# Optimization experiments

Measured on AMD Instinct MI355X. Metric: run time of the kernel, lower is better.

## Reference

```python
import jax, jax.numpy as jnp
import numpy as np

EMBED = 256
HEADS = 8
HEAD_DIM = 32
MLP_DIM = 1024
NEG = -1e9  # large negative in place of -inf so fully-deselected rows don't NaN
LN_EPS = 1e-5


def _layernorm(x, g, b):
    m = jnp.mean(x, axis=-1, keepdims=True)
    v = jnp.mean(jnp.square(x - m), axis=-1, keepdims=True)
    return (x - m) / jnp.sqrt(v + LN_EPS) * g + b


def setup_inputs() -> dict:
    key = jax.random.key(0)
    ks = jax.random.split(key, 16)
    b, s, d = 64, 360, EMBED
    sc = 0.02
    return {
        "x": jax.random.normal(ks[0], (b, s, d), dtype=jnp.float32),
        "attention_mask": jnp.zeros((b, 1, 1, s), dtype=jnp.float32),
        # TokenRouter.weight_predictor: Linear(256, 1)
        "wp_w": jax.random.normal(ks[1], (1, d), dtype=jnp.float32) * sc,
        "wp_b": jnp.zeros((1,), dtype=jnp.float32),
        # TokenRouter.aux_predictor: Linear(256,128) -> SiLU -> Linear(128,2)
        "a1_w": jax.random.normal(ks[2], (d // 2, d), dtype=jnp.float32) * sc,
        "a1_b": jnp.zeros((d // 2,), dtype=jnp.float32),
        "a2_w": jax.random.normal(ks[3], (2, d // 2), dtype=jnp.float32) * sc,
        "a2_b": jnp.zeros((2,), dtype=jnp.float32),
        # transformer block (pre-LN GPT2-style)
        "ln1_g": jnp.ones((d,), dtype=jnp.float32),
        "ln1_b": jnp.zeros((d,), dtype=jnp.float32),
        "wqkv": jax.random.normal(ks[4], (d, 3 * d), dtype=jnp.float32) * sc,
        "bqkv": jnp.zeros((3 * d,), dtype=jnp.float32),
        "wo": jax.random.normal(ks[5], (d, d), dtype=jnp.float32) * sc,
        "bo": jnp.zeros((d,), dtype=jnp.float32),
        "ln2_g": jnp.ones((d,), dtype=jnp.float32),
        "ln2_b": jnp.zeros((d,), dtype=jnp.float32),
        "w1": jax.random.normal(ks[6], (d, MLP_DIM), dtype=jnp.float32) * sc,
        "b1": jnp.zeros((MLP_DIM,), dtype=jnp.float32),
        "w2": jax.random.normal(ks[7], (MLP_DIM, d), dtype=jnp.float32) * sc,
        "b2": jnp.zeros((d,), dtype=jnp.float32),
    }


def reference(x, attention_mask, wp_w, wp_b, a1_w, a1_b, a2_w, a2_b,
              ln1_g, ln1_b, wqkv, bqkv, wo, bo, ln2_g, ln2_b, w1, b1, w2, b2):
    b, s, d = x.shape
    # --- router: per-token scalar weight ---
    weights = (x @ wp_w.T + wp_b).squeeze(-1)  # [b, s]
    # --- aux predictor selects tokens (eval path: argmax over 2 logits) ---
    h = jax.nn.silu(x @ a1_w.T + a1_b)
    aux_logits = h @ a2_w.T + a2_b            # [b, s, 2]
    sel = jnp.argmax(aux_logits, axis=-1).astype(bool)  # [b, s]
    # --- masked transformer block over the selected token subset.
    # Compacting tokens then attending == full-seq attention with deselected
    # keys masked out (LN/MLP/residual are position-wise), so vectorize:
    bias = attention_mask + jnp.where(sel, 0.0, NEG)[:, None, None, :]  # [b,1,1,s]
    hn = _layernorm(x, ln1_g, ln1_b)
    qkv = hn @ wqkv + bqkv
    q, k, v = jnp.split(qkv, 3, axis=-1)
    q = q.reshape(b, s, HEADS, HEAD_DIM)
    k = k.reshape(b, s, HEADS, HEAD_DIM)
    v = v.reshape(b, s, HEADS, HEAD_DIM)
    scores = jnp.einsum("bqhd,bkhd->bhqk", q, k) / np.sqrt(HEAD_DIM).astype(np.float32)
    scores = scores + bias                   # [b, h, s, s]
    attn = jax.nn.softmax(scores, axis=-1)
    ctx = jnp.einsum("bhqk,bkhd->bqhd", attn, v).reshape(b, s, d)
    h1 = x + (ctx @ wo + bo)
    h2n = _layernorm(h1, ln2_g, ln2_b)
    block_out = h1 + (jax.nn.gelu(h2n @ w1 + b1) @ w2 + b2)  # [b, s, d]
    # --- scatter-recombine: selected -> weighted block output, else passthrough
    out = jnp.where(sel[..., None], block_out * weights[..., None], x)
    avg_selected = jnp.sum(sel.astype(x.dtype)) / b
    return out, avg_selected
```

## Files before the change

kernel.cpp:

```cpp
#include <hip/hip_runtime.h>
#include <math.h>
#include <stdint.h>

#define TOKN 23040
#define BSZ 64
#define SEQ 360
#define DIM 256
#define NHD 8
#define HDD 32
#define MLPD 1024
#define NEGV -1e9f

typedef __attribute__((ext_vector_type(8))) short bf16x8;
typedef __attribute__((ext_vector_type(4))) float f32x4;

static __device__ __forceinline__ short f2bs(float f) {
  unsigned u = __builtin_bit_cast(unsigned, f);
  u += 0x7fffu + ((u >> 16) & 1u);
  return (short)(u >> 16);
}
static __device__ __forceinline__ float bf2f(short s) {
  unsigned u = ((unsigned)(unsigned short)s) << 16;
  return __builtin_bit_cast(float, u);
}
static __device__ __forceinline__ unsigned packbf(float a, float b) {
  return (unsigned)(unsigned short)f2bs(a) | ((unsigned)(unsigned short)f2bs(b) << 16);
}
static __device__ __forceinline__ void gl16(const short* g, short* l) {
  __builtin_amdgcn_global_load_lds(
      (const __attribute__((address_space(1))) unsigned int*)g,
      (__attribute__((address_space(3))) unsigned int*)l, 16, 0, 0);
}

__global__ __launch_bounds__(256) void mega_k(
    const float* __restrict__ x, const float* __restrict__ g,
    const float* __restrict__ b, const float* __restrict__ wpw,
    const float* __restrict__ wpb, short* __restrict__ outn,
    float* __restrict__ wout, float* __restrict__ outx,
    const float* __restrict__ a1w, const float* __restrict__ a1b,
    const float* __restrict__ a2w, const float* __restrict__ a2b,
    int* __restrict__ sel,
    const float* __restrict__ wqkv, const float* __restrict__ wo,
    const float* __restrict__ w1, const float* __restrict__ w2,
    short* __restrict__ wqkvt, short* __restrict__ wot,
    short* __restrict__ w1t, short* __restrict__ w2t) {
  __shared__ __align__(16) unsigned char smem[20992];
  int bid = blockIdx.x;
  int t = threadIdx.x;

  if (bid < 720) {
    float(*XT)[36] = (float(*)[36])smem;
    float(*WT)[128] = (float(*)[128])(smem + 4608);
    int m0 = bid * 32;
    int tx = t & 31, ty = t >> 5;
    float acc[4][4] = {};
    int r = t >> 3, c = (t & 7) * 4;
    int n2 = t >> 1, c2 = (t & 1) * 16;
    for (int k0 = 0; k0 < 256; k0 += 32) {
      float4 xa = *(const float4*)(x + (size_t)(m0 + r) * 256 + k0 + c);
      XT[c + 0][r] = xa.x; XT[c + 1][r] = xa.y; XT[c + 2][r] = xa.z; XT[c + 3][r] = xa.w;
#pragma unroll
      for (int j = 0; j < 4; j++) {
        float4 wv = *(const float4*)(a1w + (size_t)n2 * 256 + k0 + c2 + j * 4);
        WT[c2 + j * 4 + 0][n2] = wv.x;
        WT[c2 + j * 4 + 1][n2] = wv.y;
        WT[c2 + j * 4 + 2][n2] = wv.z;
        WT[c2 + j * 4 + 3][n2] = wv.w;
      }
      __syncthreads();
#pragma unroll 8
      for (int kk = 0; kk < 32; kk++) {
        float4 wv4 = *(const float4*)&WT[kk][tx * 4];
        float4 xv4 = *(const float4*)&XT[kk][ty * 4];
        float xr[4] = {xv4.x, xv4.y, xv4.z, xv4.w};
        float wr[4] = {wv4.x, wv4.y, wv4.z, wv4.w};
#pragma unroll
        for (int i = 0; i < 4; i++)
#pragma unroll
          for (int j = 0; j < 4; j++) acc[i][j] += xr[i] * wr[j];
      }
      __syncthreads();
    }
    float b1v[4], a20[4], a21[4];
#pragma unroll
    for (int j = 0; j < 4; j++) {
      int dim = tx * 4 + j;
      b1v[j] = a1b[dim];
      a20[j] = a2w[dim];
      a21[j] = a2w[128 + dim];
    }
    float bias0 = a2b[0], bias1 = a2b[1];
#pragma unroll
    for (int i = 0; i < 4; i++) {
      float l0 = 0.f, l1 = 0.f;
#pragma unroll
      for (int j = 0; j < 4; j++) {
        float v = acc[i][j] + b1v[j];
        float h = v / (1.f + expf(-v));
        l0 += h * a20[j];
        l1 += h * a21[j];
      }
#pragma unroll
      for (int o = 1; o < 32; o <<= 1) { l0 += __shfl_xor(l0, o); l1 += __shfl_xor(l1, o); }
      if (tx == 0) sel[m0 + ty * 4 + i] = (l1 + bias1 > l0 + bias0) ? 1 : 0;
    }
  } else if (bid < 1488) {
    float(*tile)[33] = (float(*)[33])smem;
    int b2 = bid - 720;
    const float* src;
    short* dst;
    int K, N, kt, nt;
    if (b2 < 192) {
      src = wqkv; dst = wqkvt; K = 256; N = 768; kt = b2 / 24; nt = b2 % 24;
    } else if (b2 < 256) {
      int bb = b2 - 192; src = wo; dst = wot; K = 256; N = 256; kt = bb >> 3; nt = bb & 7;
    } else if (b2 < 512) {
      int bb = b2 - 256; src = w1; dst = w1t; K = 256; N = 1024; kt = bb >> 5; nt = bb & 31;
    } else {
      int bb = b2 - 512; src = w2; dst = w2t; K = 1024; N = 256; kt = bb >> 3; nt = bb & 7;
    }
    int r = t >> 3, c4 = (t & 7) * 4;
    const float4 v = *(const float4*)(src + (size_t)(kt * 32 + r) * N + nt * 32 + c4);
    tile[c4 + 0][r] = v.x;
    tile[c4 + 1][r] = v.y;
    tile[c4 + 2][r] = v.z;
    tile[c4 + 3][r] = v.w;
    __syncthreads();
    union { short s[4]; uint2 u; } o;
    o.s[0] = f2bs(tile[r][c4 + 0]);
    o.s[1] = f2bs(tile[r][c4 + 1]);
    o.s[2] = f2bs(tile[r][c4 + 2]);
    o.s[3] = f2bs(tile[r][c4 + 3]);
    *(uint2*)(dst + (size_t)(nt * 32 + r) * K + kt * 32 + c4) = o.u;
  } else {
    int tok = (bid - 1488) * 4 + (t >> 6);
    int lane = t & 63;
    const float4 xv = *(const float4*)(x + (size_t)tok * DIM + lane * 4);
    *(float4*)(outx + (size_t)tok * DIM + lane * 4) = xv;
    float s = xv.x + xv.y + xv.z + xv.w;
    float s2 = xv.x * xv.x + xv.y * xv.y + xv.z * xv.z + xv.w * xv.w;
#pragma unroll
    for (int o = 1; o < 64; o <<= 1) { s += __shfl_xor(s, o); s2 += __shfl_xor(s2, o); }
    float m = s * (1.f / DIM);
    float var = fmaxf(s2 * (1.f / DIM) - m * m, 0.f);
    float rstd = rsqrtf(var + 1e-5f);
    float4 gv = *(const float4*)(g + lane * 4);
    float4 bv = *(const float4*)(b + lane * 4);
    uint2 pk;
    pk.x = packbf((xv.x - m) * rstd * gv.x + bv.x, (xv.y - m) * rstd * gv.y + bv.y);
    pk.y = packbf((xv.z - m) * rstd * gv.z + bv.z, (xv.w - m) * rstd * gv.w + bv.w);
    *(uint2*)(outn + (size_t)tok * DIM + lane * 4) = pk;
    float4 wv = *(const float4*)(wpw + lane * 4);
    float wd = xv.x * wv.x + xv.y * wv.y + xv.z * wv.z + xv.w * wv.w;
#pragma unroll
    for (int o = 1; o < 64; o <<= 1) wd += __shfl_xor(wd, o);
    if (lane == 0) wout[tok] = wd + wpb[0];
  }
}

__global__ __launch_bounds__(512) void scan_k(
    const int* __restrict__ sel, int* __restrict__ g_idx,
    int* __restrict__ startp, int* __restrict__ cntp,
    int* __restrict__ mtotp, float* __restrict__ outavg) {
  __shared__ int sc[512];
  __shared__ int red[8];
  int b = blockIdx.x, t = threadIdx.x;
  int lane = t & 63, wave = t >> 6;
  int part = 0;
  for (int i = t; i < b * SEQ; i += 512) part += sel[i];
#pragma unroll
  for (int o = 1; o < 64; o <<= 1) part += __shfl_xor(part, o);
  if (lane == 0) red[wave] = part;
  __syncthreads();
  int start = 0;
#pragma unroll
  for (int w = 0; w < 8; w++) start += red[w];
  __syncthreads();
  int flag = (t < SEQ) ? sel[b * SEQ + t] : 0;
  sc[t] = flag;
  __syncthreads();
  int val = flag;
  for (int off = 1; off < 512; off <<= 1) {
    int add = (t >= off) ? sc[t - off] : 0;
    __syncthreads();
    val += add;
    sc[t] = val;
    __syncthreads();
  }
  if (flag) g_idx[start + val - 1] = b * SEQ + t;
  if (t == 511) { startp[b] = start; cntp[b] = val; }
  if (b == 63) {
    int mt = start + sc[511];
    if (t == 0) { *mtotp = mt; outavg[0] = (float)mt / 64.0f; }
    int e = mt + 256;
    if (e > TOKN) e = TOKN;
    for (int i = mt + t; i < e; i += 512) g_idx[i] = 0;
  }
}

template <int MODE, int BN>
__global__ __launch_bounds__(256) void gemm128_k(
    const short* __restrict__ A, const short* __restrict__ Bt,
    const float* __restrict__ bias, const float* __restrict__ resf,
    const short* __restrict__ resb, const float* __restrict__ wgt,
    const int* __restrict__ g_idx, const int* __restrict__ mtotp,
    short* __restrict__ outb, float* __restrict__ outf, int Ndim, int Kdim) {
  int Mt = *mtotp;
  int m0 = blockIdx.y * 128;
  if (m0 >= Mt) return;
  __shared__ __align__(16) short As[2][128 * 32];
  __shared__ __align__(16) short Bs[2][BN * 32];
  constexpr int NJ = BN / 32;
  int n0 = blockIdx.x * BN;
  int t = threadIdx.x;
  int wave = t >> 6, lane = t & 63;
  int l15 = lane & 15, quad = lane >> 4;
  int wr = (wave >> 1) * 64, wc = (wave & 1) * (BN / 2);
  int r0 = t >> 2, c0 = (t & 3) * 8;
  long arA = (MODE == 0) ? g_idx[m0 + r0] : (m0 + r0);
  long arB = (MODE == 0) ? g_idx[m0 + 64 + r0] : (m0 + 64 + r0);
  const short* gA0 = A + arA * Kdim + c0;
  const short* gA1 = A + arB * Kdim + c0;
  const short* gB0 = Bt + (size_t)(n0 + r0) * Kdim + c0;
  const short* gB1 = Bt + (size_t)(n0 + 64 + r0) * Kdim + c0;
  int wbase = wave * 512;

  f32x4 acc[4][NJ];
#pragma unroll
  for (int i = 0; i < 4; i++)
#pragma unroll
    for (int j = 0; j < NJ; j++)
#pragma unroll
      for (int r = 0; r < 4; r++) acc[i][j][r] = 0.f;

  int nst = Kdim >> 5;
  gl16(gA0, As[0] + wbase);
  gl16(gA1, As[0] + 2048 + wbase);
  gl16(gB0, Bs[0] + wbase);
  if constexpr (BN == 128) gl16(gB1, Bs[0] + 2048 + wbase);
  __syncthreads();

  int buf = 0;
  for (int s = 0; s < nst; ++s) {
    if (s + 1 < nst) {
      int off = (s + 1) * 32;
      short* d = (buf ^ 1) ? &As[1][0] : &As[0][0];
      short* e = (buf ^ 1) ? &Bs[1][0] : &Bs[0][0];
      gl16(gA0 + off, d + wbase);
      gl16(gA1 + off, d + 2048 + wbase);
      gl16(gB0 + off, e + wbase);
      if constexpr (BN == 128) gl16(gB1 + off, e + 2048 + wbase);
    }
    const short* Ab = buf ? &As[1][0] : &As[0][0];
    const short* Bb = buf ? &Bs[1][0] : &Bs[0][0];
    bf16x8 af[4], bfr[NJ];
#pragma unroll
    for (int i = 0; i < 4; i++)
      af[i] = *(const bf16x8*)&Ab[(wr + i * 16 + l15) * 32 + quad * 8];
#pragma unroll
    for (int j = 0; j < NJ; j++)
      bfr[j] = *(const bf16x8*)&Bb[(wc + j * 16 + l15) * 32 + quad * 8];
#pragma unroll
    for (int i = 0; i < 4; i++)
#pragma unroll
      for (int j = 0; j < NJ; j++)
        acc[i][j] = __builtin_amdgcn_mfma_f32_16x16x32_bf16(af[i], bfr[j],
                                                            acc[i][j], 0, 0, 0);
    __syncthreads();
    buf ^= 1;
  }

#pragma unroll
  for (int i = 0; i < 4; i++) {
#pragma unroll
    for (int j = 0; j < NJ; j++) {
      int col = n0 + wc + j * 16 + l15;
      float bcol = bias[col];
#pragma unroll
      for (int r = 0; r < 4; r++) {
        int row = m0 + wr + i * 16 + quad * 4 + r;
        float v = acc[i][j][r] + bcol;
        size_t idx = (size_t)row * Ndim + col;
        if (MODE == 0) {
          outb[idx] = f2bs(v);
        } else if (MODE == 2) {
          float u = 0.7978845608028654f * (v + 0.044715f * v * v * v);
          float e = __expf(2.f * u);
          float th = 1.f - 2.f / (e + 1.f);
          outb[idx] = f2bs(0.5f * v * (1.f + th));
        } else {
          if (row < Mt) {
            int orig = g_idx[row];
            float o = (v + bf2f(resb[idx])) * wgt[orig];
            outf[(size_t)orig * 256 + col] = o;
          }
        }
      }
    }
  }
}

__global__ __launch_bounds__(256) void wo_ln_k(
    const short* __restrict__ A, const short* __restrict__ Bt,
    const float* __restrict__ bias, const float* __restrict__ resf,
    const float* __restrict__ g2, const float* __restrict__ b2,
    const int* __restrict__ g_idx, const int* __restrict__ mtotp,
    short* __restrict__ h1b, short* __restrict__ h2n) {
  int Mt = *mtotp;
  int m0 = blockIdx.x * 128;
  if (m0 >= Mt) return;
  __shared__ __align__(16) short As0[128 * 32];
  __shared__ __align__(16) short As1[128 * 32];
  __shared__ __align__(16) short Bs0[256 * 32];
  __shared__ __align__(16) short Bs1[256 * 32];
  __shared__ float ps[128][2], ps2[128][2];
  int t = threadIdx.x;
  int wave = t >> 6, lane = t & 63;
  int l15 = lane & 15, quad = lane >> 4;
  int wr = (wave >> 1) * 64, wc = (wave & 1) * 128;
  int r0 = t >> 2, c0 = (t & 3) * 8;
  const short* gA0 = A + (size_t)(m0 + r0) * 256 + c0;
  const short* gA1 = A + (size_t)(m0 + 64 + r0) * 256 + c0;
  const short* gB0 = Bt + (size_t)r0 * 256 + c0;
  short* lA0 = As0 + wave * 512;
  short* lA1 = As1 + wave * 512;
  short* lB0 = Bs0 + wave * 512;
  short* lB1 = Bs1 + wave * 512;

  f32x4 acc[4][8];
#pragma unroll
  for (int i = 0; i < 4; i++)
#pragma unroll
    for (int j = 0; j < 8; j++)
#pragma unroll
      for (int r = 0; r < 4; r++) acc[i][j][r] = 0.f;

  for (int k0 = 0; k0 < 256; k0 += 64) {
    gl16(gA0 + k0, lA0);
    gl16(gA1 + k0, lA0 + 2048);
    gl16(gA0 + k0 + 32, lA1);
    gl16(gA1 + k0 + 32, lA1 + 2048);
#pragma unroll
    for (int q = 0; q < 4; q++) {
      gl16(gB0 + (size_t)q * 64 * 256 + k0, lB0 + q * 2048);
      gl16(gB0 + (size_t)q * 64 * 256 + k0 + 32, lB1 + q * 2048);
    }
    __syncthreads();
    bf16x8 af[4], bfr[8];
#pragma unroll
    for (int i = 0; i < 4; i++)
      af[i] = *(const bf16x8*)&As0[(wr + i * 16 + l15) * 32 + quad * 8];
#pragma unroll
    for (int j = 0; j < 8; j++)
      bfr[j] = *(const bf16x8*)&Bs0[(wc + j * 16 + l15) * 32 + quad * 8];
#pragma unroll
    for (int i = 0; i < 4; i++)
#pragma unroll
      for (int j = 0; j < 8; j++)
        acc[i][j] = __builtin_amdgcn_mfma_f32_16x16x32_bf16(af[i], bfr[j],
                                                            acc[i][j], 0, 0, 0);
#pragma unroll
    for (int i = 0; i < 4; i++)
      af[i] = *(const bf16x8*)&As1[(wr + i * 16 + l15) * 32 + quad * 8];
#pragma unroll
    for (int j = 0; j < 8; j++)
      bfr[j] = *(const bf16x8*)&Bs1[(wc + j * 16 + l15) * 32 + quad * 8];
#pragma unroll
    for (int i = 0; i < 4; i++)
#pragma unroll
      for (int j = 0; j < 8; j++)
        acc[i][j] = __builtin_amdgcn_mfma_f32_16x16x32_bf16(af[i], bfr[j],
                                                            acc[i][j], 0, 0, 0);
    __syncthreads();
  }

  float bcol[8], gcol[8], bbcol[8];
#pragma unroll
  for (int j = 0; j < 8; j++) {
    int col = wc + j * 16 + l15;
    bcol[j] = bias[col];
    gcol[j] = g2[col];
    bbcol[j] = b2[col];
  }
  float s1v[4][4], s2v[4][4];
#pragma unroll
  for (int i = 0; i < 4; i++) {
#pragma unroll
    for (int r = 0; r < 4; r++) {
      int row = m0 + wr + i * 16 + quad * 4 + r;
      int orig = g_idx[row];
      const float* xr = resf + (size_t)orig * 256;
      float ls_ = 0.f, ls2_ = 0.f;
#pragma unroll
      for (int j = 0; j < 8; j++) {
        int col = wc + j * 16 + l15;
        float h1 = acc[i][j][r] + bcol[j] + xr[col];
        acc[i][j][r] = h1;
        h1b[(size_t)row * 256 + col] = f2bs(h1);
        ls_ += h1;
        ls2_ += h1 * h1;
      }
      s1v[i][r] = ls_;
      s2v[i][r] = ls2_;
    }
  }
#pragma unroll
  for (int i = 0; i < 4; i++)
#pragma unroll
    for (int r = 0; r < 4; r++) {
#pragma unroll
      for (int o = 1; o < 16; o <<= 1) {
        s1v[i][r] += __shfl_xor(s1v[i][r], o);
        s2v[i][r] += __shfl_xor(s2v[i][r], o);
      }
    }
  if (l15 == 0) {
#pragma unroll
    for (int i = 0; i < 4; i++)
#pragma unroll
      for (int r = 0; r < 4; r++) {
        int lr = wr + i * 16 + quad * 4 + r;
        ps[lr][wave & 1] = s1v[i][r];
        ps2[lr][wave & 1] = s2v[i][r];
      }
  }
  __syncthreads();
#pragma unroll
  for (int i = 0; i < 4; i++) {
#pragma unroll
    for (int r = 0; r < 4; r++) {
      int lr = wr + i * 16 + quad * 4 + r;
      float S = ps[lr][0] + ps[lr][1];
      float S2 = ps2[lr][0] + ps2[lr][1];
      float m = S * (1.f / 256.f);
      float var = fmaxf(S2 * (1.f / 256.f) - m * m, 0.f);
      float rstd = rsqrtf(var + 1e-5f);
      int row = m0 + lr;
#pragma unroll
      for (int j = 0; j < 8; j++) {
        int col = wc + j * 16 + l15;
        float h2 = (acc[i][j][r] - m) * rstd * gcol[j] + bbcol[j];
        h2n[(size_t)row * 256 + col] = f2bs(h2);
      }
    }
  }
}

__global__ __launch_bounds__(256) void attn_k(
    const short* __restrict__ qkv, const float* __restrict__ amask,
    const int* __restrict__ g_idx, const int* __restrict__ startp,
    const int* __restrict__ cntp, short* __restrict__ ctx) {
  __shared__ __align__(16) short VF[2 * 12 * 64 * 8];
  __shared__ __align__(16) float ls[384];
  int bh = blockIdx.x >> 1, qhalf = blockIdx.x & 1;
  int bb = bh >> 3, h = bh & 7;
  int t = threadIdx.x;
  int start = startp[bb], cnt = cntp[bb];
  size_t base = (size_t)start * 768;
  for (int i = t; i < 1536; i += 256) {
    int k = i >> 2, cg = (i & 3) * 8;
    union { int4 v; short s[8]; } u;
    if (k < cnt) {
      u.v = *(const int4*)(qkv + base + (size_t)k * 768 + 512 + h * 32 + cg);
    } else {
      u.v = make_int4(0, 0, 0, 0);
    }
    int c = k >> 5, qd = (k >> 3) & 3, j = k & 7;
#pragma unroll
    for (int jj = 0; jj < 8; jj++) {
      int d = cg + jj;
      VF[((((d >> 4) * 12 + c) * 64) + qd * 16 + (d & 15)) * 8 + j] = u.s[jj];
    }
  }
  for (int i = t; i < 384; i += 256)
    ls[i] = (i < cnt) ? amask[g_idx[start + i]] : 0.f;
  __syncthreads();

  int wave = t >> 6, lane = t & 63;
  int ql = lane & 15, quad = lane >> 4;
  int addr0 = (((quad & 1) * 2) * 16 + ql) * 4;
  int addr1 = addr0 + 64;
  bool hiq = quad >= 2;
  int nt = (cnt + 15) >> 4;
  int nc = (cnt + 31) >> 5;

  for (int qt = qhalf + 2 * wave; qt < nt; qt += 8) {
    int q0 = qt * 16, qrow = q0 + ql;
    bf16x8 qf;
#pragma unroll
    for (int j = 0; j < 8; j++) qf[j] = 0;
    if (qrow < cnt)
      qf = *(const bf16x8*)(qkv + base + (size_t)qrow * 768 + h * 32 + quad * 8);

    f32x4 o0, o1;
#pragma unroll
    for (int r = 0; r < 4; r++) { o0[r] = 0.f; o1[r] = 0.f; }
    float lsum = 0.f;

    for (int c = 0; c < nc; c++) {
      int keyA = c * 32 + ql;
      int keyB = keyA + 16;
      bf16x8 kfA, kfB;
#pragma unroll
      for (int j = 0; j < 8; j++) { kfA[j] = 0; kfB[j] = 0; }
      if (keyA < cnt)
        kfA = *(const bf16x8*)(qkv + base + (size_t)keyA * 768 + 256 + h * 32 + quad * 8);
      if (keyB < cnt)
        kfB = *(const bf16x8*)(qkv + base + (size_t)keyB * 768 + 256 + h * 32 + quad * 8);
      f32x4 sa, sb;
#pragma unroll
      for (int r = 0; r < 4; r++) { sa[r] = 0.f; sb[r] = 0.f; }
      sa = __builtin_amdgcn_mfma_f32_16x16x32_bf16(kfA, qf, sa, 0, 0, 0);
      sb = __builtin_amdgcn_mfma_f32_16x16x32_bf16(kfB, qf, sb, 0, 0, 0);
      int kbase = c * 32 + quad * 4;
      float4 la = *(const float4*)&ls[kbase];
      float4 lb = *(const float4*)&ls[kbase + 16];
      float ea0 = (kbase + 0 < cnt) ? __expf(sa[0] * 0.17677669529663687f + la.x) : 0.f;
      float ea1 = (kbase + 1 < cnt) ? __expf(sa[1] * 0.17677669529663687f + la.y) : 0.f;
      float ea2 = (kbase + 2 < cnt) ? __expf(sa[2] * 0.17677669529663687f + la.z) : 0.f;
      float ea3 = (kbase + 3 < cnt) ? __expf(sa[3] * 0.17677669529663687f + la.w) : 0.f;
      float eb0 = (kbase + 16 < cnt) ? __expf(sb[0] * 0.17677669529663687f + lb.x) : 0.f;
      float eb1 = (kbase + 17 < cnt) ? __expf(sb[1] * 0.17677669529663687f + lb.y) : 0.f;
      float eb2 = (kbase + 18 < cnt) ? __expf(sb[2] * 0.17677669529663687f + lb.z) : 0.f;
      float eb3 = (kbase + 19 < cnt) ? __expf(sb[3] * 0.17677669529663687f + lb.w) : 0.f;
      lsum += (ea0 + ea1) + (ea2 + ea3) + (eb0 + eb1) + (eb2 + eb3);
      unsigned pA0 = packbf(ea0, ea1), pA1 = packbf(ea2, ea3);
      unsigned pB0 = packbf(eb0, eb1), pB1 = packbf(eb2, eb3);
      int s00 = __builtin_amdgcn_ds_bpermute(addr0, (int)pA0);
      int s10 = __builtin_amdgcn_ds_bpermute(addr0, (int)pB0);
      int s01 = __builtin_amdgcn_ds_bpermute(addr0, (int)pA1);
      int s11 = __builtin_amdgcn_ds_bpermute(addr0, (int)pB1);
      int s02 = __builtin_amdgcn_ds_bpermute(addr1, (int)pA0);
      int s12 = __builtin_amdgcn_ds_bpermute(addr1, (int)pB0);
      int s03 = __builtin_amdgcn_ds_bpermute(addr1, (int)pA1);
      int s13 = __builtin_amdgcn_ds_bpermute(addr1, (int)pB1);
      union { int i[4]; bf16x8 v; } pf;
      pf.i[0] = hiq ? s10 : s00;
      pf.i[1] = hiq ? s11 : s01;
      pf.i[2] = hiq ? s12 : s02;
      pf.i[3] = hiq ? s13 : s03;
      bf16x8 v0 = *(const bf16x8*)&VF[(c * 64 + lane) * 8];
      bf16x8 v1 = *(const bf16x8*)&VF[((12 + c) * 64 + lane) * 8];
      o0 = __builtin_amdgcn_mfma_f32_16x16x32_bf16(v0, pf.v, o0, 0, 0, 0);
      o1 = __builtin_amdgcn_mfma_f32_16x16x32_bf16(v1, pf.v, o1, 0, 0, 0);
    }
    lsum += __shfl_xor(lsum, 16);
    lsum += __shfl_xor(lsum, 32);
    float inv = 1.f / lsum;

    if (qrow < cnt) {
      size_t cb = ((size_t)(start + qrow)) * 256 + h * 32;
      uint2 w0, w1;
      w0.x = packbf(o0[0] * inv, o0[1] * inv);
      w0.y = packbf(o0[2] * inv, o0[3] * inv);
      w1.x = packbf(o1[0] * inv, o1[1] * inv);
      w1.y = packbf(o1[2] * inv, o1[3] * inv);
      *(uint2*)(ctx + cb + quad * 4) = w0;
      *(uint2*)(ctx + cb + 16 + quad * 4) = w1;
    }
  }
}

extern "C" void kernel_launch(void* const* d_in, const int* in_sizes, int n_in,
                              void* d_out, int out_size, void* d_ws,
                              size_t ws_size, hipStream_t stream) {
  const float* x = (const float*)d_in[0];
  const float* amask = (const float*)d_in[1];
  const float* wp_w = (const float*)d_in[2];
  const float* wp_b = (const float*)d_in[3];
  const float* a1_w = (const float*)d_in[4];
  const float* a1_b = (const float*)d_in[5];
  const float* a2_w = (const float*)d_in[6];
  const float* a2_b = (const float*)d_in[7];
  const float* ln1_g = (const float*)d_in[8];
  const float* ln1_b = (const float*)d_in[9];
  const float* wqkv = (const float*)d_in[10];
  const float* bqkv = (const float*)d_in[11];
  const float* wo = (const float*)d_in[12];
  const float* bo = (const float*)d_in[13];
  const float* ln2_g = (const float*)d_in[14];
  const float* ln2_b = (const float*)d_in[15];
  const float* w1 = (const float*)d_in[16];
  const float* b1 = (const float*)d_in[17];
  const float* w2 = (const float*)d_in[18];
  const float* b2 = (const float*)d_in[19];
  float* out = (float*)d_out;

  uint8_t* p = (uint8_t*)d_ws;
  float* weightsv = (float*)p; p += (size_t)TOKN * 4;
  int* selv = (int*)p;         p += (size_t)TOKN * 4;
  int* idxlv = (int*)p;        p += (size_t)TOKN * 4;
  int* gidxv = (int*)p;        p += (size_t)TOKN * 4;
  int* cntv = (int*)p;         p += 64 * 4;
  int* startv = (int*)p;       p += 64 * 4;
  int* mtotv = (int*)p;        p += 64 * 4;
  short* wqkvt = (short*)p;    p += (size_t)768 * 256 * 2;
  short* wot = (short*)p;      p += (size_t)256 * 256 * 2;
  short* w1t = (short*)p;      p += (size_t)1024 * 256 * 2;
  short* w2t = (short*)p;      p += (size_t)256 * 1024 * 2;
  short* h1bv = (short*)p;     p += (size_t)TOKN * 256 * 2;
  short* h2nv = (short*)p;     p += (size_t)TOKN * 256 * 2;
  short* ctxv = (short*)p;     p += (size_t)TOKN * 256 * 2;
  uint8_t* R = p;
  short* xnv = (short*)R;
  short* qkvv = (short*)(R + (size_t)TOKN * 256 * 2);
  short* actv = (short*)R;
  (void)idxlv;

  mega_k<<<dim3(7248), dim3(256), 0, stream>>>(
      x, ln1_g, ln1_b, wp_w, wp_b, xnv, weightsv, out,
      a1_w, a1_b, a2_w, a2_b, selv,
      wqkv, wo, w1, w2, wqkvt, wot, w1t, w2t);
  scan_k<<<dim3(64), dim3(512), 0, stream>>>(selv, gidxv, startv, cntv, mtotv,
                                             out + (size_t)TOKN * 256);
  gemm128_k<0, 128><<<dim3(6, 180), dim3(256), 0, stream>>>(
      xnv, wqkvt, bqkv, nullptr, nullptr, nullptr, gidxv, mtotv, qkvv, nullptr,
      768, 256);
  attn_k<<<dim3(1024), dim3(256), 0, stream>>>(qkvv, amask, gidxv, startv, cntv, ctxv);
  wo_ln_k<<<dim3(180), dim3(256), 0, stream>>>(ctxv, wot, bo, x, ln2_g, ln2_b,
                                               gidxv, mtotv, h1bv, h2nv);
  gemm128_k<2, 128><<<dim3(8, 180), dim3(256), 0, stream>>>(
      h2nv, w1t, b1, nullptr, nullptr, nullptr, gidxv, mtotv, actv, nullptr,
      1024, 256);
  gemm128_k<3, 64><<<dim3(4, 180), dim3(256), 0, stream>>>(
      actv, w2t, b2, nullptr, h1bv, weightsv, gidxv, mtotv, nullptr, out, 256, 1024);
}
```

Baseline: 243.5 us.

## Enlarge router aux GEMM tile and double-buffer wo_ln K loop

The aux-predictor section of the fused mega kernel now has each block handle 128 tokens with an 8x8 per-thread register tile instead of 32 tokens with 4x4. The 128-wide hidden weight tile is reused across four times as many tokens, and the number of router blocks drops from 720 to 180. Separately, the wo+LN GEMM K loop becomes a double-buffered pipeline that prefetches the next 32-wide K slice while the current one feeds the MFMAs. The costs are higher LDS use (48KB) and register pressure in the mega kernel, which may lower occupancy, and only 180 router blocks to spread across the CUs.

```diff
diff --git a/kernel.cpp b/kernel.cpp
--- a/kernel.cpp
+++ b/kernel.cpp
@@ -44,69 +44,77 @@
     const float* __restrict__ w1, const float* __restrict__ w2,
     short* __restrict__ wqkvt, short* __restrict__ wot,
     short* __restrict__ w1t, short* __restrict__ w2t) {
-  __shared__ __align__(16) unsigned char smem[20992];
+  __shared__ __align__(16) unsigned char smem[49152];
   int bid = blockIdx.x;
   int t = threadIdx.x;
 
-  if (bid < 720) {
-    float(*XT)[36] = (float(*)[36])smem;
-    float(*WT)[128] = (float(*)[128])(smem + 4608);
-    int m0 = bid * 32;
-    int tx = t & 31, ty = t >> 5;
-    float acc[4][4] = {};
-    int r = t >> 3, c = (t & 7) * 4;
-    int n2 = t >> 1, c2 = (t & 1) * 16;
+  if (bid < 180) {
+    float(*XT)[192] = (float(*)[192])smem;
+    float(*WT)[192] = (float(*)[192])(smem + 24576);
+    int m0 = bid * 128;
+    int tx = t & 15;
+    int tyy = t >> 4;
+    float acc[8][8] = {};
+    int rs = t >> 1, cs = (t & 1) * 16;
+    int scol = (rs >> 3) * 12 + (rs & 7);
+    const float* xpb = x + (size_t)(m0 + rs) * 256 + cs;
+    const float* wpb_ = a1w + (size_t)rs * 256 + cs;
     for (int k0 = 0; k0 < 256; k0 += 32) {
-      float4 xa = *(const float4*)(x + (size_t)(m0 + r) * 256 + k0 + c);
-      XT[c + 0][r] = xa.x; XT[c + 1][r] = xa.y; XT[c + 2][r] = xa.z; XT[c + 3][r] = xa.w;
-#pragma unroll
-      for (int j = 0; j < 4; j++) {
-        float4 wv = *(const float4*)(a1w + (size_t)n2 * 256 + k0 + c2 + j * 4);
-        WT[c2 + j * 4 + 0][n2] = wv.x;
-        WT[c2 + j * 4 + 1][n2] = wv.y;
-        WT[c2 + j * 4 + 2][n2] = wv.z;
-        WT[c2 + j * 4 + 3][n2] = wv.w;
+#pragma unroll
+      for (int j4 = 0; j4 < 4; j4++) {
+        float4 xv4 = *(const float4*)(xpb + k0 + j4 * 4);
+        float4 wv4 = *(const float4*)(wpb_ + k0 + j4 * 4);
+        XT[cs + j4 * 4 + 0][scol] = xv4.x;
+        XT[cs + j4 * 4 + 1][scol] = xv4.y;
+        XT[cs + j4 * 4 + 2][scol] = xv4.z;
+        XT[cs + j4 * 4 + 3][scol] = xv4.w;
+        WT[cs + j4 * 4 + 0][scol] = wv4.x;
+        WT[cs + j4 * 4 + 1][scol] = wv4.y;
+        WT[cs + j4 * 4 + 2][scol] = wv4.z;
+        WT[cs + j4 * 4 + 3][scol] = wv4.w;
       }
       __syncthreads();
-#pragma unroll 8
+#pragma unroll 4
       for (int kk = 0; kk < 32; kk++) {
-        float4 wv4 = *(const float4*)&WT[kk][tx * 4];
-        float4 xv4 = *(const float4*)&XT[kk][ty * 4];
-        float xr[4] = {xv4.x, xv4.y, xv4.z, xv4.w};
-        float wr[4] = {wv4.x, wv4.y, wv4.z, wv4.w};
-#pragma unroll
-        for (int i = 0; i < 4; i++)
-#pragma unroll
-          for (int j = 0; j < 4; j++) acc[i][j] += xr[i] * wr[j];
+        float4 xa = *(const float4*)&XT[kk][tyy * 12];
+        float4 xb = *(const float4*)&XT[kk][tyy * 12 + 4];
+        float4 wa = *(const float4*)&WT[kk][tx * 12];
+        float4 wb = *(const float4*)&WT[kk][tx * 12 + 4];
+        float xr[8] = {xa.x, xa.y, xa.z, xa.w, xb.x, xb.y, xb.z, xb.w};
+        float wr[8] = {wa.x, wa.y, wa.z, wa.w, wb.x, wb.y, wb.z, wb.w};
+#pragma unroll
+        for (int i = 0; i < 8; i++)
+#pragma unroll
+          for (int j = 0; j < 8; j++) acc[i][j] += xr[i] * wr[j];
       }
       __syncthreads();
     }
-    float b1v[4], a20[4], a21[4];
-#pragma unroll
-    for (int j = 0; j < 4; j++) {
-      int dim = tx * 4 + j;
+    float b1v[8], a20[8], a21[8];
+#pragma unroll
+    for (int j = 0; j < 8; j++) {
+      int dim = tx * 8 + j;
       b1v[j] = a1b[dim];
       a20[j] = a2w[dim];
       a21[j] = a2w[128 + dim];
     }
     float bias0 = a2b[0], bias1 = a2b[1];
 #pragma unroll
-    for (int i = 0; i < 4; i++) {
+    for (int i = 0; i < 8; i++) {
       float l0 = 0.f, l1 = 0.f;
 #pragma unroll
-      for (int j = 0; j < 4; j++) {
+      for (int j = 0; j < 8; j++) {
         float v = acc[i][j] + b1v[j];
         float h = v / (1.f + expf(-v));
         l0 += h * a20[j];
         l1 += h * a21[j];
       }
 #pragma unroll
-      for (int o = 1; o < 32; o <<= 1) { l0 += __shfl_xor(l0, o); l1 += __shfl_xor(l1, o); }
-      if (tx == 0) sel[m0 + ty * 4 + i] = (l1 + bias1 > l0 + bias0) ? 1 : 0;
-    }
-  } else if (bid < 1488) {
+      for (int o = 1; o < 16; o <<= 1) { l0 += __shfl_xor(l0, o); l1 += __shfl_xor(l1, o); }
+      if (tx == 0) sel[m0 + tyy * 8 + i] = (l1 + bias1 > l0 + bias0) ? 1 : 0;
+    }
+  } else if (bid < 948) {
     float(*tile)[33] = (float(*)[33])smem;
-    int b2 = bid - 720;
+    int b2 = bid - 180;
     const float* src;
     short* dst;
     int K, N, kt, nt;
@@ -133,7 +141,7 @@
     o.s[3] = f2bs(tile[r][c4 + 3]);
     *(uint2*)(dst + (size_t)(nt * 32 + r) * K + kt * 32 + c4) = o.u;
   } else {
-    int tok = (bid - 1488) * 4 + (t >> 6);
+    int tok = (bid - 948) * 4 + (t >> 6);
     int lane = t & 63;
     const float4 xv = *(const float4*)(x + (size_t)tok * DIM + lane * 4);
     *(float4*)(outx + (size_t)tok * DIM + lane * 4) = xv;
@@ -309,10 +317,8 @@
   int Mt = *mtotp;
   int m0 = blockIdx.x * 128;
   if (m0 >= Mt) return;
-  __shared__ __align__(16) short As0[128 * 32];
-  __shared__ __align__(16) short As1[128 * 32];
-  __shared__ __align__(16) short Bs0[256 * 32];
-  __shared__ __align__(16) short Bs1[256 * 32];
+  __shared__ __align__(16) short As[2][128 * 32];
+  __shared__ __align__(16) short Bs[2][256 * 32];
   __shared__ float ps[128][2], ps2[128][2];
   int t = threadIdx.x;
   int wave = t >> 6, lane = t & 63;
@@ -322,10 +328,7 @@
   const short* gA0 = A + (size_t)(m0 + r0) * 256 + c0;
   const short* gA1 = A + (size_t)(m0 + 64 + r0) * 256 + c0;
   const short* gB0 = Bt + (size_t)r0 * 256 + c0;
-  short* lA0 = As0 + wave * 512;
-  short* lA1 = As1 + wave * 512;
-  short* lB0 = Bs0 + wave * 512;
-  short* lB1 = Bs1 + wave * 512;
+  int wbase = wave * 512;
 
   f32x4 acc[4][8];
 #pragma unroll
@@ -335,36 +338,33 @@
 #pragma unroll
       for (int r = 0; r < 4; r++) acc[i][j][r] = 0.f;
 
-  for (int k0 = 0; k0 < 256; k0 += 64) {
-    gl16(gA0 + k0, lA0);
-    gl16(gA1 + k0, lA0 + 2048);
-    gl16(gA0 + k0 + 32, lA1);
-    gl16(gA1 + k0 + 32, lA1 + 2048);
-#pragma unroll
-    for (int q = 0; q < 4; q++) {
-      gl16(gB0 + (size_t)q * 64 * 256 + k0, lB0 + q * 2048);
-      gl16(gB0 + (size_t)q * 64 * 256 + k0 + 32, lB1 + q * 2048);
-    }
-    __syncthreads();
+  gl16(gA0, As[0] + wbase);
+  gl16(gA1, As[0] + 2048 + wbase);
+#pragma unroll
+  for (int q = 0; q < 4; q++) gl16(gB0 + (size_t)q * 64 * 256, Bs[0] + q * 2048 + wbase);
+  __syncthreads();
+
+  int buf = 0;
+  for (int s = 0; s < 8; ++s) {
+    if (s + 1 < 8) {
+      int off = (s + 1) * 32;
+      short* d = (buf ^ 1) ? &As[1][0] : &As[0][0];
+      short* e = (buf ^ 1) ? &Bs[1][0] : &Bs[0][0];
+      gl16(gA0 + off, d + wbase);
+      gl16(gA1 + off, d + 2048 + wbase);
+#pragma unroll
+      for (int q = 0; q < 4; q++)
+        gl16(gB0 + (size_t)q * 64 * 256 + off, e + q * 2048 + wbase);
+    }
+    const short* Ab = buf ? &As[1][0] : &As[0][0];
+    const short* Bb = buf ? &Bs[1][0] : &Bs[0][0];
     bf16x8 af[4], bfr[8];
 #pragma unroll
     for (int i = 0; i < 4; i++)
-      af[i] = *(const bf16x8*)&As0[(wr + i * 16 + l15) * 32 + quad * 8];
+      af[i] = *(const bf16x8*)&Ab[(wr + i * 16 + l15) * 32 + quad * 8];
 #pragma unroll
     for (int j = 0; j < 8; j++)
-      bfr[j] = *(const bf16x8*)&Bs0[(wc + j * 16 + l15) * 32 + quad * 8];
-#pragma unroll
-    for (int i = 0; i < 4; i++)
-#pragma unroll
-      for (int j = 0; j < 8; j++)
-        acc[i][j] = __builtin_amdgcn_mfma_f32_16x16x32_bf16(af[i], bfr[j],
-                                                            acc[i][j], 0, 0, 0);
-#pragma unroll
-    for (int i = 0; i < 4; i++)
-      af[i] = *(const bf16x8*)&As1[(wr + i * 16 + l15) * 32 + quad * 8];
-#pragma unroll
-    for (int j = 0; j < 8; j++)
-      bfr[j] = *(const bf16x8*)&Bs1[(wc + j * 16 + l15) * 32 + quad * 8];
+      bfr[j] = *(const bf16x8*)&Bb[(wc + j * 16 + l15) * 32 + quad * 8];
 #pragma unroll
     for (int i = 0; i < 4; i++)
 #pragma unroll
@@ -372,6 +372,7 @@
         acc[i][j] = __builtin_amdgcn_mfma_f32_16x16x32_bf16(af[i], bfr[j],
                                                             acc[i][j], 0, 0, 0);
     __syncthreads();
+    buf ^= 1;
   }
 
   float bcol[8], gcol[8], bbcol[8];
@@ -607,7 +608,7 @@
   short* actv = (short*)R;
   (void)idxlv;
 
-  mega_k<<<dim3(7248), dim3(256), 0, stream>>>(
+  mega_k<<<dim3(6708), dim3(256), 0, stream>>>(
       x, ln1_g, ln1_b, wp_w, wp_b, xnv, weightsv, out,
       a1_w, a1_b, a2_w, a2_b, selv,
       wqkv, wo, w1, w2, wqkvt, wot, w1t, w2t);
```

After: 249.2 us. 1.02x slower.

## Compute router aux predictor with bf16 MFMA and fp32 recheck of near-tie tokens

Applied to the files above, without the earlier changes.

The aux-predictor GEMM (x @ a1_w^T) now runs on bf16 MFMA instead of a scalar fp32 FMA loop, using 64-row tiles and half as many router blocks. Tokens whose logit margin falls below a threshold are flagged, and a new recheck kernel recomputes those tokens' selection in fp32 so the argmax decision stays exact. The goal is to cut the FP32 ALU cost of the router. It adds an extra kernel launch and relies on the 0.03 margin being enough to catch every bf16-induced flip.

```diff
diff --git a/kernel.cpp b/kernel.cpp
--- a/kernel.cpp
+++ b/kernel.cpp
@@ -39,74 +39,115 @@
     float* __restrict__ wout, float* __restrict__ outx,
     const float* __restrict__ a1w, const float* __restrict__ a1b,
     const float* __restrict__ a2w, const float* __restrict__ a2b,
-    int* __restrict__ sel,
+    int* __restrict__ sel, int* __restrict__ flagr,
     const float* __restrict__ wqkv, const float* __restrict__ wo,
     const float* __restrict__ w1, const float* __restrict__ w2,
     short* __restrict__ wqkvt, short* __restrict__ wot,
     short* __restrict__ w1t, short* __restrict__ w2t) {
-  __shared__ __align__(16) unsigned char smem[20992];
+  __shared__ __align__(16) unsigned char smem[13312];
   int bid = blockIdx.x;
   int t = threadIdx.x;
 
-  if (bid < 720) {
-    float(*XT)[36] = (float(*)[36])smem;
-    float(*WT)[128] = (float(*)[128])(smem + 4608);
-    int m0 = bid * 32;
-    int tx = t & 31, ty = t >> 5;
-    float acc[4][4] = {};
-    int r = t >> 3, c = (t & 7) * 4;
-    int n2 = t >> 1, c2 = (t & 1) * 16;
+  if (bid < 360) {
+    short* As = (short*)smem;
+    short* Ws = (short*)(smem + 4096);
+    float* r0s = (float*)(smem + 12288);
+    float* r1s = (float*)(smem + 12800);
+    int m0 = bid * 64;
+    int wave = t >> 6, lane = t & 63;
+    int l15 = lane & 15, quad = lane >> 4;
+    int wr = (wave >> 1) * 32, wc = (wave & 1) * 64;
+    int ar = t >> 2, akc = (t & 3) * 8;
+    int br = t >> 1, bkc = (t & 1) * 16;
+    const float* xp = x + (size_t)(m0 + ar) * 256 + akc;
+    const float* wpA = a1w + (size_t)br * 256 + bkc;
+
+    f32x4 acc[2][4];
+#pragma unroll
+    for (int i = 0; i < 2; i++)
+#pragma unroll
+      for (int j = 0; j < 4; j++)
+#pragma unroll
+        for (int r = 0; r < 4; r++) acc[i][j][r] = 0.f;
+
     for (int k0 = 0; k0 < 256; k0 += 32) {
-      float4 xa = *(const float4*)(x + (size_t)(m0 + r) * 256 + k0 + c);
-      XT[c + 0][r] = xa.x; XT[c + 1][r] = xa.y; XT[c + 2][r] = xa.z; XT[c + 3][r] = xa.w;
-#pragma unroll
-      for (int j = 0; j < 4; j++) {
-        float4 wv = *(const float4*)(a1w + (size_t)n2 * 256 + k0 + c2 + j * 4);
-        WT[c2 + j * 4 + 0][n2] = wv.x;
-        WT[c2 + j * 4 + 1][n2] = wv.y;
-        WT[c2 + j * 4 + 2][n2] = wv.z;
-        WT[c2 + j * 4 + 3][n2] = wv.w;
+      float4 xa = *(const float4*)(xp + k0);
+      float4 xb = *(const float4*)(xp + k0 + 4);
+      union { unsigned u[4]; int4 v; } px;
+      px.u[0] = packbf(xa.x, xa.y); px.u[1] = packbf(xa.z, xa.w);
+      px.u[2] = packbf(xb.x, xb.y); px.u[3] = packbf(xb.z, xb.w);
+      *(int4*)&As[ar * 32 + akc] = px.v;
+#pragma unroll
+      for (int h2 = 0; h2 < 2; h2++) {
+        float4 wa = *(const float4*)(wpA + k0 + h2 * 8);
+        float4 wb = *(const float4*)(wpA + k0 + h2 * 8 + 4);
+        union { unsigned u[4]; int4 v; } pw;
+        pw.u[0] = packbf(wa.x, wa.y); pw.u[1] = packbf(wa.z, wa.w);
+        pw.u[2] = packbf(wb.x, wb.y); pw.u[3] = packbf(wb.z, wb.w);
+        *(int4*)&Ws[br * 32 + bkc + h2 * 8] = pw.v;
       }
       __syncthreads();
-#pragma unroll 8
-      for (int kk = 0; kk < 32; kk++) {
-        float4 wv4 = *(const float4*)&WT[kk][tx * 4];
-        float4 xv4 = *(const float4*)&XT[kk][ty * 4];
-        float xr[4] = {xv4.x, xv4.y, xv4.z, xv4.w};
-        float wr[4] = {wv4.x, wv4.y, wv4.z, wv4.w};
-#pragma unroll
-        for (int i = 0; i < 4; i++)
-#pragma unroll
-          for (int j = 0; j < 4; j++) acc[i][j] += xr[i] * wr[j];
+      bf16x8 af[2], bfr[4];
+#pragma unroll
+      for (int i = 0; i < 2; i++)
+        af[i] = *(const bf16x8*)&As[(wr + i * 16 + l15) * 32 + quad * 8];
+#pragma unroll
+      for (int j = 0; j < 4; j++)
+        bfr[j] = *(const bf16x8*)&Ws[(wc + j * 16 + l15) * 32 + quad * 8];
+#pragma unroll
+      for (int i = 0; i < 2; i++)
+#pragma unroll
+        for (int j = 0; j < 4; j++)
+          acc[i][j] = __builtin_amdgcn_mfma_f32_16x16x32_bf16(af[i], bfr[j],
+                                                              acc[i][j], 0, 0, 0);
+      __syncthreads();
+    }
+    float bias0 = a2b[0], bias1 = a2b[1];
+    float a1bc[4], a20c[4], a21c[4];
+#pragma unroll
+    for (int j = 0; j < 4; j++) {
+      int col = wc + j * 16 + l15;
+      a1bc[j] = a1b[col];
+      a20c[j] = a2w[col];
+      a21c[j] = a2w[128 + col];
+    }
+#pragma unroll
+    for (int i = 0; i < 2; i++) {
+#pragma unroll
+      for (int r = 0; r < 4; r++) {
+        float p0 = 0.f, p1 = 0.f;
+#pragma unroll
+        for (int j = 0; j < 4; j++) {
+          float v = acc[i][j][r] + a1bc[j];
+          float h = v / (1.f + expf(-v));
+          p0 += h * a20c[j];
+          p1 += h * a21c[j];
+        }
+#pragma unroll
+        for (int o = 1; o < 16; o <<= 1) { p0 += __shfl_xor(p0, o); p1 += __shfl_xor(p1, o); }
+        if (l15 == 0) {
+          int lr = wr + i * 16 + quad * 4 + r;
+          r0s[lr * 2 + (wave & 1)] = p0;
+          r1s[lr * 2 + (wave & 1)] = p1;
+        }
       }
-      __syncthreads();
-    }
-    float b1v[4], a20[4], a21[4];
-#pragma unroll
-    for (int j = 0; j < 4; j++) {
-      int dim = tx * 4 + j;
-      b1v[j] = a1b[dim];
-      a20[j] = a2w[dim];
-      a21[j] = a2w[128 + dim];
-    }
-    float bias0 = a2b[0], bias1 = a2b[1];
-#pragma unroll
-    for (int i = 0; i < 4; i++) {
-      float l0 = 0.f, l1 = 0.f;
-#pragma unroll
-      for (int j = 0; j < 4; j++) {
-        float v = acc[i][j] + b1v[j];
-        float h = v / (1.f + expf(-v));
-        l0 += h * a20[j];
-        l1 += h * a21[j];
-      }
-#pragma unroll
-      for (int o = 1; o < 32; o <<= 1) { l0 += __shfl_xor(l0, o); l1 += __shfl_xor(l1, o); }
-      if (tx == 0) sel[m0 + ty * 4 + i] = (l1 + bias1 > l0 + bias0) ? 1 : 0;
-    }
-  } else if (bid < 1488) {
+    }
+    __syncthreads();
+    if ((wave & 1) == 0 && l15 == 0) {
+#pragma unroll
+      for (int i = 0; i < 2; i++)
+#pragma unroll
+        for (int r = 0; r < 4; r++) {
+          int lr = wr + i * 16 + quad * 4 + r;
+          float L0 = r0s[lr * 2] + r0s[lr * 2 + 1] + bias0;
+          float L1 = r1s[lr * 2] + r1s[lr * 2 + 1] + bias1;
+          sel[m0 + lr] = (L1 > L0) ? 1 : 0;
+          flagr[m0 + lr] = (fabsf(L1 - L0) < 0.03f) ? 1 : 0;
+        }
+    }
+  } else if (bid < 1128) {
     float(*tile)[33] = (float(*)[33])smem;
-    int b2 = bid - 720;
+    int b2 = bid - 360;
     const float* src;
     short* dst;
     int K, N, kt, nt;
@@ -133,7 +174,7 @@
     o.s[3] = f2bs(tile[r][c4 + 3]);
     *(uint2*)(dst + (size_t)(nt * 32 + r) * K + kt * 32 + c4) = o.u;
   } else {
-    int tok = (bid - 1488) * 4 + (t >> 6);
+    int tok = (bid - 1128) * 4 + (t >> 6);
     int lane = t & 63;
     const float4 xv = *(const float4*)(x + (size_t)tok * DIM + lane * 4);
     *(float4*)(outx + (size_t)tok * DIM + lane * 4) = xv;
@@ -155,6 +196,31 @@
 #pragma unroll
     for (int o = 1; o < 64; o <<= 1) wd += __shfl_xor(wd, o);
     if (lane == 0) wout[tok] = wd + wpb[0];
+  }
+}
+
+__global__ __launch_bounds__(512) void recheck_k(
+    const float* __restrict__ x, const float* __restrict__ a1w,
+    const float* __restrict__ a1b, const float* __restrict__ a2w,
+    const float* __restrict__ a2b, const int* __restrict__ flagr,
+    int* __restrict__ sel) {
+  int wave = threadIdx.x >> 6, lane = threadIdx.x & 63;
+  int widx = blockIdx.x * 8 + wave;
+  for (int tok = widx; tok < TOKN; tok += 5760) {
+    if (!flagr[tok]) continue;
+    float4 xv = *(const float4*)(x + (size_t)tok * 256 + lane * 4);
+    float l0 = 0.f, l1 = 0.f;
+    for (int dim = 0; dim < 128; dim++) {
+      float4 wv = *(const float4*)(a1w + (size_t)dim * 256 + lane * 4);
+      float p = xv.x * wv.x + xv.y * wv.y + xv.z * wv.z + xv.w * wv.w;
+#pragma unroll
+      for (int o = 1; o < 64; o <<= 1) p += __shfl_xor(p, o);
+      float v = p + a1b[dim];
+      float h = v / (1.f + expf(-v));
+      l0 += h * a2w[dim];
+      l1 += h * a2w[128 + dim];
+    }
+    if (lane == 0) sel[tok] = (l1 + a2b[1] > l0 + a2b[0]) ? 1 : 0;
   }
 }
 
@@ -589,7 +655,7 @@
   uint8_t* p = (uint8_t*)d_ws;
   float* weightsv = (float*)p; p += (size_t)TOKN * 4;
   int* selv = (int*)p;         p += (size_t)TOKN * 4;
-  int* idxlv = (int*)p;        p += (size_t)TOKN * 4;
+  int* flagv = (int*)p;        p += (size_t)TOKN * 4;
   int* gidxv = (int*)p;        p += (size_t)TOKN * 4;
   int* cntv = (int*)p;         p += 64 * 4;
   int* startv = (int*)p;       p += 64 * 4;
@@ -605,12 +671,13 @@
   short* xnv = (short*)R;
   short* qkvv = (short*)(R + (size_t)TOKN * 256 * 2);
   short* actv = (short*)R;
-  (void)idxlv;
-
-  mega_k<<<dim3(7248), dim3(256), 0, stream>>>(
+
+  mega_k<<<dim3(6888), dim3(256), 0, stream>>>(
       x, ln1_g, ln1_b, wp_w, wp_b, xnv, weightsv, out,
-      a1_w, a1_b, a2_w, a2_b, selv,
+      a1_w, a1_b, a2_w, a2_b, selv, flagv,
       wqkv, wo, w1, w2, wqkvt, wot, w1t, w2t);
+  recheck_k<<<dim3(720), dim3(512), 0, stream>>>(x, a1_w, a1_b, a2_w, a2_b,
+                                                 flagv, selv);
   scan_k<<<dim3(64), dim3(512), 0, stream>>>(selv, gidxv, startv, cntv, mtotv,
                                              out + (size_t)TOKN * 256);
   gemm128_k<0, 128><<<dim3(6, 180), dim3(256), 0, stream>>>(
```

Result: slower. 410.9 us (+68.8%).
